# Performance work log

Measured on AMD Instinct MI355X. Metric: run time of the kernel, lower is better.

Reference implementation:

```python
import jax, jax.numpy as jnp
import numpy as np

N_NODES = 8192
N_EDGES = 65536
MUL = 16          # multiplicity of 0e and 1o irreps
NB = 16           # num_radial_basis
HID = 16          # num_radial_dimension
MAX_RADIUS = 5.0
SQRT3 = float(np.sqrt(3.0))


def soft_unit_step(x):
    # e3nn.math.soft_unit_step: exp(-1/x) for x>0 else 0 (grad-safe where)
    safe = jnp.where(x > 0, x, 1.0)
    return jnp.where(x > 0, jnp.exp(-1.0 / safe), 0.0)


def setup_inputs() -> dict:
    key = jax.random.key(0)
    ks = jax.random.split(key, 12)
    f_in = jax.random.normal(ks[0], (N_NODES, 4 * MUL), jnp.float32)
    edge_vec = jax.random.normal(ks[1], (N_EDGES, 3), jnp.float32) * 1.5
    edge_src = jax.random.randint(ks[2], (N_EDGES,), 0, N_NODES)
    edge_dst = jax.random.randint(ks[3], (N_EDGES,), 0, N_NODES)
    Wq0 = jax.random.normal(ks[4], (MUL, MUL), jnp.float32)
    Wq1 = jax.random.normal(ks[5], (MUL, MUL), jnp.float32)
    Wk1 = jax.random.normal(ks[6], (NB, HID), jnp.float32)
    Wk2 = jax.random.normal(ks[7], (HID, 4 * MUL * MUL), jnp.float32)
    Wv1 = jax.random.normal(ks[8], (NB, HID), jnp.float32)
    Wv2 = jax.random.normal(ks[9], (HID, 4 * MUL * MUL), jnp.float32)
    Wd0 = jax.random.normal(ks[10], (MUL, MUL), jnp.float32)
    Wd1 = jax.random.normal(ks[11], (MUL, MUL), jnp.float32)
    return dict(f_in=f_in, edge_vec=edge_vec, edge_src=edge_src, edge_dst=edge_dst,
                Wq0=Wq0, Wq1=Wq1, Wk1=Wk1, Wk2=Wk2, Wv1=Wv1, Wv2=Wv2, Wd0=Wd0, Wd1=Wd1)


def _forward(f_in, edge_vec, edge_src, edge_dst,
             Wq0, Wq1, Wk1, Wk2, Wv1, Wv2, Wd0, Wd1):
    f0 = f_in[:, :MUL]                         # [N, MUL]    0e scalars
    f1 = f_in[:, MUL:].reshape(-1, MUL, 3)     # [N, MUL, 3] 1o vectors

    r = jnp.linalg.norm(edge_vec, axis=1)      # [E]
    u = edge_vec / r[:, None]
    sh1 = SQRT3 * u                            # Y_1, component norm (|Y1|^2 = 3); Y_0 = 1

    # soft_one_hot_linspace, basis='smooth_finite', cutoff=True, * sqrt(NB)
    values = jnp.linspace(0.0, MAX_RADIUS, NB + 2)
    step = values[1] - values[0]
    diff = (r[:, None] - values[1:-1]) / step
    C = 1.14136 * float(np.exp(2.0))
    rb = (C * soft_unit_step(diff + 1.0) * soft_unit_step(1.0 - diff)) * np.sqrt(NB)

    edge_cut = soft_unit_step(10.0 * (1.0 - r / MAX_RADIUS))  # [E]

    def mlp(x, W1, W2):  # e3nn FullyConnectedNet with fan-in normalization
        h = jax.nn.silu(x @ (W1 / np.sqrt(NB)))
        return h @ (W2 / np.sqrt(HID))

    wk = mlp(rb, Wk1, Wk2).reshape(-1, 4, MUL, MUL)  # per-edge TP weights
    wv = mlp(rb, Wv1, Wv2).reshape(-1, 4, MUL, MUL)

    # h_q: per-irrep linear
    q0 = f0 @ Wq0 / np.sqrt(MUL)
    q1 = jnp.einsum('nic,io->noc', f1, Wq1) / np.sqrt(MUL)

    x0 = f0[edge_src]   # [E, MUL]
    x1 = f1[edge_src]   # [E, MUL, 3]

    def fctp(w):
        # FullyConnectedTensorProduct (16x0e+16x1o) x (0e+1o) -> (16x0e+16x1o)
        # 4 paths: 0x0->0, 1x1->0 (dot/sqrt3), 0x1->1, 1x0->1
        a = 1.0 / np.sqrt(2 * MUL)
        o0 = jnp.einsum('eij,ei->ej', w[:, 0], x0) \
           + jnp.einsum('eij,eic,ec->ej', w[:, 1], x1, sh1) / SQRT3
        o1 = jnp.einsum('eij,ei,ec->ejc', w[:, 2], x0, sh1) \
           + jnp.einsum('eij,eic->ejc', w[:, 3], x1)
        return o0 * a, o1 * a

    k0, k1 = fctp(wk)
    v0, v1 = fctp(wv)

    # dot_product: FCTP(query, key) -> 0e
    ad = 1.0 / np.sqrt(2.0 * MUL * MUL)
    dot = ad * (jnp.einsum('ij,ei,ej->e', Wd0, q0[edge_dst], k0)
                + jnp.einsum('ij,eic,ejc->e', Wd1, q1[edge_dst], k1) / SQRT3)

    exp = edge_cut * jnp.exp(dot)                                   # [E]
    z = jax.ops.segment_sum(exp, edge_dst, num_segments=N_NODES)    # [N]
    z = jnp.where(z == 0.0, 1.0, z)
    alpha = exp / z[edge_dst]
    # alpha.relu().sqrt() with grad-safe sqrt at 0
    s = jnp.where(alpha > 0, jnp.sqrt(jnp.where(alpha > 0, alpha, 1.0)), 0.0)

    f_out0 = jax.ops.segment_sum(s[:, None] * v0, edge_dst, num_segments=N_NODES)
    f_out1 = jax.ops.segment_sum(s[:, None, None] * v1, edge_dst, num_segments=N_NODES)
    return jnp.concatenate([f_out0, f_out1.reshape(-1, MUL * 3)], axis=-1)  # [N, 64]


def reference(f_in, edge_vec, edge_src, edge_dst,
              Wq0, Wq1, Wk1, Wk2, Wv1, Wv2, Wd0, Wd1):
    return _forward(f_in, edge_vec, edge_src, edge_dst,
                    Wq0, Wq1, Wk1, Wk2, Wv1, Wv2, Wd0, Wd1)
```

## Files before the change

kernel.cpp:

```cpp
#include <hip/hip_runtime.h>
#include <hip/hip_bf16.h>

#define N_NODES 8192
#define N_EDGES 65536

#define CNT_OFF  0
#define RP_OFF   8192
#define WF_OFF   16640
#define QD0_OFF  33024
#define QD1_OFF  164096
#define EXP_OFF  557312
#define VH_OFF   622848

typedef _Float16 half8 __attribute__((ext_vector_type(8)));
typedef float f32x4 __attribute__((ext_vector_type(4)));

__device__ __forceinline__ float sus_f(float x) { return x > 0.f ? expf(-1.f / x) : 0.f; }
__device__ __forceinline__ float silu_f(float x) { return x / (1.f + expf(-x)); }

__device__ __forceinline__ half8 vmul(half8 v, _Float16 s) {
    half8 r;
#pragma unroll
    for (int d = 0; d < 8; ++d) r[d] = v[d] * s;
    return r;
}

__global__ __launch_bounds__(256) void k_prep(
    const float* __restrict__ f_in,
    const float* __restrict__ Wq0, const float* __restrict__ Wq1,
    const float* __restrict__ Wd0, const float* __restrict__ Wd1,
    const float* __restrict__ Wk2, const float* __restrict__ Wv2,
    const int* __restrict__ edst,
    half8* __restrict__ wfrag, float* __restrict__ qd0, float* __restrict__ qd1,
    int* __restrict__ cnt) {
    __shared__ float f0s[16][16];
    __shared__ float f1s[16][48];
    __shared__ float t0s[16][16];
    __shared__ float t1s[16][48];
    const int blk = blockIdx.x;
    const int tid = threadIdx.x;

    if (blk < 16) {
        int g = blk * 256 + tid;
        int lane = g & 63, t = (g >> 6) & 7, b = (g >> 9) & 3, kv = g >> 11;
        const float* src = kv ? Wv2 : Wk2;
        int n = lane & 15, quad = lane >> 4;
        const float SC = 0.044194173824159216f;
        half8 out;
#pragma unroll
        for (int d = 0; d < 8; ++d) {
            int k = t * 32 + quad * 8 + d;
            int i = k & 15, h = k >> 4;
            out[d] = (_Float16)(src[h * 1024 + b * 256 + i * 16 + n] * SC);
        }
        wfrag[g] = out;
        return;
    }
    if (blk >= 528) {
        int base = (blk - 528) * 256 + tid;
#pragma unroll
        for (int k = 0; k < 4; ++k) atomicAdd(cnt + edst[base + k * 16384], 1);
        return;
    }
    const int j = tid & 15, ln = tid >> 4;
    const int n = (blk - 16) * 16 + ln;
    f0s[ln][j]         = f_in[n * 64 + j];
    f1s[ln][j * 3 + 0] = f_in[n * 64 + 16 + j * 3 + 0];
    f1s[ln][j * 3 + 1] = f_in[n * 64 + 16 + j * 3 + 1];
    f1s[ln][j * 3 + 2] = f_in[n * 64 + 16 + j * 3 + 2];
    __syncthreads();
    float t0 = 0.f, ta = 0.f, tb = 0.f, tc = 0.f;
#pragma unroll
    for (int p = 0; p < 16; ++p) {
        float wq0 = Wq0[p * 16 + j];
        float wq1 = Wq1[p * 16 + j];
        t0 += f0s[ln][p] * wq0;
        ta += f1s[ln][p * 3 + 0] * wq1;
        tb += f1s[ln][p * 3 + 1] * wq1;
        tc += f1s[ln][p * 3 + 2] * wq1;
    }
    t0s[ln][j] = t0;
    t1s[ln][j * 3 + 0] = ta; t1s[ln][j * 3 + 1] = tb; t1s[ln][j * 3 + 2] = tc;
    __syncthreads();
    float q0a = 0.f, qa = 0.f, qb = 0.f, qc = 0.f;
#pragma unroll
    for (int i = 0; i < 16; ++i) {
        float wd0 = Wd0[i * 16 + j];
        float wd1 = Wd1[i * 16 + j];
        q0a += t0s[ln][i] * wd0;
        qa  += t1s[ln][i * 3 + 0] * wd1;
        qb  += t1s[ln][i * 3 + 1] * wd1;
        qc  += t1s[ln][i * 3 + 2] * wd1;
    }
    const float S0 = 0.011048543456f;
    const float S1 = 0.0063788674817f;
    qd0[n * 16 + j] = q0a * S0;
    qd1[0 * 131072 + n * 16 + j] = qa * S1;
    qd1[1 * 131072 + n * 16 + j] = qb * S1;
    qd1[2 * 131072 + n * 16 + j] = qc * S1;
}

__global__ __launch_bounds__(1024) void k_scan(int* __restrict__ cnt, int* __restrict__ rowptr) {
    __shared__ int wsum[16];
    __shared__ int woff[16];
    const int t = threadIdx.x;
    const int lane = t & 63, wv = t >> 6;
    const int base = t * 8;
    int v[8]; int s = 0;
    int4 p0 = ((const int4*)cnt)[t * 2];
    int4 p1 = ((const int4*)cnt)[t * 2 + 1];
    v[0] = p0.x; v[1] = p0.y; v[2] = p0.z; v[3] = p0.w;
    v[4] = p1.x; v[5] = p1.y; v[6] = p1.z; v[7] = p1.w;
#pragma unroll
    for (int i = 0; i < 8; ++i) s += v[i];
    int own = s;
#pragma unroll
    for (int off = 1; off < 64; off <<= 1) {
        int u = __shfl_up(s, off);
        if (lane >= off) s += u;
    }
    if (lane == 63) wsum[wv] = s;
    __syncthreads();
    if (wv == 0 && lane < 16) {
        int u = wsum[lane];
        int sc = u;
#pragma unroll
        for (int off = 1; off < 16; off <<= 1) {
            int x = __shfl_up(sc, off);
            if (lane >= off) sc += x;
        }
        woff[lane] = sc - u;
    }
    __syncthreads();
    int run = woff[wv] + (s - own);
#pragma unroll
    for (int i = 0; i < 8; ++i) { rowptr[base + i] = run; cnt[base + i] = run; run += v[i]; }
    if (t == 1023) rowptr[8192] = run;
}

__global__ __launch_bounds__(256) void k_edge(
    const float* __restrict__ f_in, const float* __restrict__ evec,
    const int* __restrict__ esrc, const int* __restrict__ edst,
    const float* __restrict__ Wk1, const float* __restrict__ Wv1,
    const half8* __restrict__ wfrag,
    const float* __restrict__ qd0, const float* __restrict__ qd1,
    int* __restrict__ cursor, float* __restrict__ expbuf, _Float16* __restrict__ vh) {
    __shared__ __align__(16) char s_arena[19456];
    _Float16 (*s_x0h)[24] = (_Float16(*)[24])(s_arena);
    _Float16 (*s_xsh)[24] = (_Float16(*)[24])(s_arena + 3072);
    _Float16 (*s_x1h0)[24] = (_Float16(*)[24])(s_arena + 6144);
    _Float16 (*s_x1h1)[24] = (_Float16(*)[24])(s_arena + 9216);
    _Float16 (*s_x1h2)[24] = (_Float16(*)[24])(s_arena + 12288);
    _Float16 (*s_hkh)[16] = (_Float16(*)[16])(s_arena + 15360);
    _Float16 (*s_hvh)[16] = (_Float16(*)[16])(s_arena + 17408);
    _Float16 (*s_vt)[72]  = (_Float16(*)[72])(s_arena);
    __shared__ float s_rb[64][16];
    __shared__ float s_sh[64][4];
    __shared__ int   s_slot[64];

    const int tid = threadIdx.x;
    const int e0 = blockIdx.x * 64;

    {
        const int el = tid >> 2, q = tid & 3;
        const int e = e0 + el;
        float v0 = evec[e * 3 + 0];
        float v1 = evec[e * 3 + 1];
        float v2 = evec[e * 3 + 2];
        float r = sqrtf(v0 * v0 + v1 * v1 + v2 * v2);
        float rs = r * 3.4f;
#pragma unroll
        for (int bb = 0; bb < 4; ++bb) {
            int b = q * 4 + bb;
            s_rb[el][b] = 33.734292f * sus_f(rs - (float)b) * sus_f((float)(b + 2) - rs);
        }
        if (q == 0) {
            float inv = r > 0.f ? 1.f / r : 0.f;
            const float SQ3 = 1.7320508075688772f;
            s_sh[el][0] = SQ3 * v0 * inv;
            s_sh[el][1] = SQ3 * v1 * inv;
            s_sh[el][2] = SQ3 * v2 * inv;
            s_sh[el][3] = sus_f(10.f - 2.f * r);
        }
    }
    __syncthreads();

    {
        const int j = tid & 15, slot = tid >> 4;
#pragma unroll
        for (int s = 0; s < 4; ++s) {
            const int el = slot * 4 + s;
            const int e = e0 + el;
            float aK = 0.f, aV = 0.f;
#pragma unroll
            for (int b = 0; b < 16; ++b) {
                float rbv = s_rb[el][b];
                aK += rbv * Wk1[b * 16 + j];
                aV += rbv * Wv1[b * 16 + j];
            }
            s_hkh[el][(j & 1) * 8 + (j >> 1)] = (_Float16)silu_f(aK * 0.25f);
            s_hvh[el][(j & 1) * 8 + (j >> 1)] = (_Float16)silu_f(aV * 0.25f);
            const int src = esrc[e];
            float x0 = f_in[src * 64 + j];
            float xa = f_in[src * 64 + 16 + j * 3 + 0];
            float xb = f_in[src * 64 + 16 + j * 3 + 1];
            float xc = f_in[src * 64 + 16 + j * 3 + 2];
            s_x0h[el][j] = (_Float16)x0;
            s_x1h0[el][j] = (_Float16)xa;
            s_x1h1[el][j] = (_Float16)xb;
            s_x1h2[el][j] = (_Float16)xc;
            s_xsh[el][j] = (_Float16)((xa * s_sh[el][0] + xb * s_sh[el][1] + xc * s_sh[el][2])
                                      * 0.57735026919f);
        }
    }
    __syncthreads();

    const int lane = tid & 63;
    const int wv = tid >> 6;
    const int m = lane & 15, quad = lane >> 4;
    const int eb = wv * 16;
    const int eloc = eb + m;
    const int ihalf = quad >> 1;
    const int hh = (quad & 1) * 8;

    half8 X0 = *(const half8*)&s_x0h[eloc][hh];
    half8 XS = *(const half8*)&s_xsh[eloc][hh];
    half8 Xa = *(const half8*)&s_x1h0[eloc][hh];
    half8 Xb = *(const half8*)&s_x1h1[eloc][hh];
    half8 Xc = *(const half8*)&s_x1h2[eloc][hh];
    half8 HK = *(const half8*)&s_hkh[eloc][ihalf * 8];
    half8 HV = *(const half8*)&s_hvh[eloc][ihalf * 8];
    __syncthreads();

    {
        f32x4 o0 = {0.f, 0.f, 0.f, 0.f}, a1 = o0, ax = o0, ay = o0, az = o0;
#pragma unroll
        for (int t = 0; t < 8; ++t) {
            _Float16 hs = HK[t];
            half8 B0 = wfrag[(0 * 8 + t) * 64 + lane];
            half8 B1 = wfrag[(1 * 8 + t) * 64 + lane];
            half8 B2 = wfrag[(2 * 8 + t) * 64 + lane];
            half8 B3 = wfrag[(3 * 8 + t) * 64 + lane];
            half8 A0 = vmul(X0, hs);
            half8 As = vmul(XS, hs);
            half8 Aa = vmul(Xa, hs);
            half8 Ab = vmul(Xb, hs);
            half8 Ac = vmul(Xc, hs);
            o0 = __builtin_amdgcn_mfma_f32_16x16x32_f16(A0, B0, o0, 0, 0, 0);
            o0 = __builtin_amdgcn_mfma_f32_16x16x32_f16(As, B1, o0, 0, 0, 0);
            a1 = __builtin_amdgcn_mfma_f32_16x16x32_f16(A0, B2, a1, 0, 0, 0);
            ax = __builtin_amdgcn_mfma_f32_16x16x32_f16(Aa, B3, ax, 0, 0, 0);
            ay = __builtin_amdgcn_mfma_f32_16x16x32_f16(Ab, B3, ay, 0, 0, 0);
            az = __builtin_amdgcn_mfma_f32_16x16x32_f16(Ac, B3, az, 0, 0, 0);
        }
        const int j = m;
#pragma unroll
        for (int r = 0; r < 4; ++r) {
            const int el = eb + quad * 4 + r;
            const int e = e0 + el;
            const int dst = edst[e];
            float sh0 = s_sh[el][0], sh1 = s_sh[el][1], sh2 = s_sh[el][2];
            float k1x = a1[r] * sh0 + ax[r];
            float k1y = a1[r] * sh1 + ay[r];
            float k1z = a1[r] * sh2 + az[r];
            float dp = qd0[dst * 16 + j] * o0[r]
                     + qd1[0 * 131072 + dst * 16 + j] * k1x
                     + qd1[1 * 131072 + dst * 16 + j] * k1y
                     + qd1[2 * 131072 + dst * 16 + j] * k1z;
            dp += __shfl_xor(dp, 1);
            dp += __shfl_xor(dp, 2);
            dp += __shfl_xor(dp, 4);
            dp += __shfl_xor(dp, 8);
            if (j == 0) {
                float ev = s_sh[el][3] * expf(dp);
                int slot = atomicAdd(cursor + dst, 1);
                s_slot[el] = slot;
                expbuf[slot] = ev;
            }
        }
    }

    {
        f32x4 o0 = {0.f, 0.f, 0.f, 0.f}, a1 = o0, ax = o0, ay = o0, az = o0;
        const half8* wfv = wfrag + 32 * 64;
#pragma unroll
        for (int t = 0; t < 8; ++t) {
            _Float16 hs = HV[t];
            half8 B0 = wfv[(0 * 8 + t) * 64 + lane];
            half8 B1 = wfv[(1 * 8 + t) * 64 + lane];
            half8 B2 = wfv[(2 * 8 + t) * 64 + lane];
            half8 B3 = wfv[(3 * 8 + t) * 64 + lane];
            half8 A0 = vmul(X0, hs);
            half8 As = vmul(XS, hs);
            half8 Aa = vmul(Xa, hs);
            half8 Ab = vmul(Xb, hs);
            half8 Ac = vmul(Xc, hs);
            o0 = __builtin_amdgcn_mfma_f32_16x16x32_f16(A0, B0, o0, 0, 0, 0);
            o0 = __builtin_amdgcn_mfma_f32_16x16x32_f16(As, B1, o0, 0, 0, 0);
            a1 = __builtin_amdgcn_mfma_f32_16x16x32_f16(A0, B2, a1, 0, 0, 0);
            ax = __builtin_amdgcn_mfma_f32_16x16x32_f16(Aa, B3, ax, 0, 0, 0);
            ay = __builtin_amdgcn_mfma_f32_16x16x32_f16(Ab, B3, ay, 0, 0, 0);
            az = __builtin_amdgcn_mfma_f32_16x16x32_f16(Ac, B3, az, 0, 0, 0);
        }
        const int j = m;
#pragma unroll
        for (int r = 0; r < 4; ++r) {
            const int el = eb + quad * 4 + r;
            float sh0 = s_sh[el][0], sh1 = s_sh[el][1], sh2 = s_sh[el][2];
            s_vt[el][j] = (_Float16)o0[r];
            s_vt[el][16 + j * 3 + 0] = (_Float16)(a1[r] * sh0 + ax[r]);
            s_vt[el][16 + j * 3 + 1] = (_Float16)(a1[r] * sh1 + ay[r]);
            s_vt[el][16 + j * 3 + 2] = (_Float16)(a1[r] * sh2 + az[r]);
        }
    }
    __syncthreads();

#pragma unroll
    for (int pass = 0; pass < 2; ++pass) {
        int row = pass * 32 + (tid >> 3);
        int part = tid & 7;
        half8 val = *(const half8*)&s_vt[row][part * 8];
        int slot = s_slot[row];
        *(half8*)(vh + (size_t)slot * 64 + part * 8) = val;
    }
}

__global__ __launch_bounds__(256) void k_out(
    const int* __restrict__ rowptr,
    const float* __restrict__ expbuf, const _Float16* __restrict__ vh,
    float* __restrict__ fout) {
    const int col = threadIdx.x & 63;
    const int n = blockIdx.x * 4 + (threadIdx.x >> 6);
    const int s0 = rowptr[n], s1 = rowptr[n + 1];
    float zs = 0.f;
    for (int p = s0 + col; p < s1; p += 64) zs += expbuf[p];
#pragma unroll
    for (int off = 32; off > 0; off >>= 1) zs += __shfl_xor(zs, off);
    float zinv = zs > 0.f ? 1.f / zs : 0.f;
    float acc = 0.f;
    for (int p = s0; p < s1; ++p) {
        float ev = expbuf[p];
        float s = ev > 0.f ? sqrtf(ev * zinv) : 0.f;
        acc += s * (float)vh[(size_t)p * 64 + col];
    }
    fout[n * 64 + col] = acc;
}

extern "C" void kernel_launch(void* const* d_in, const int* in_sizes, int n_in,
                              void* d_out, int out_size, void* d_ws, size_t ws_size,
                              hipStream_t stream) {
    const float* f_in = (const float*)d_in[0];
    const float* evec = (const float*)d_in[1];
    const int* esrc = (const int*)d_in[2];
    const int* edst = (const int*)d_in[3];
    const float* Wq0 = (const float*)d_in[4];
    const float* Wq1 = (const float*)d_in[5];
    const float* Wk1 = (const float*)d_in[6];
    const float* Wk2 = (const float*)d_in[7];
    const float* Wv1 = (const float*)d_in[8];
    const float* Wv2 = (const float*)d_in[9];
    const float* Wd0 = (const float*)d_in[10];
    const float* Wd1 = (const float*)d_in[11];

    float* ws     = (float*)d_ws;
    int*   cnt    = (int*)(ws + CNT_OFF);
    int*   rowptr = (int*)(ws + RP_OFF);
    half8* wfrag  = (half8*)(ws + WF_OFF);
    float* qd0    = ws + QD0_OFF;
    float* qd1    = ws + QD1_OFF;
    float* expb   = ws + EXP_OFF;
    _Float16* vh  = (_Float16*)(ws + VH_OFF);
    float* fout   = (float*)d_out;

    hipMemsetAsync(cnt, 0, (size_t)8192 * sizeof(int), stream);

    k_prep<<<592, 256, 0, stream>>>(f_in, Wq0, Wq1, Wd0, Wd1, Wk2, Wv2, edst,
                                    wfrag, qd0, qd1, cnt);
    k_scan<<<1, 1024, 0, stream>>>(cnt, rowptr);
    k_edge<<<N_EDGES / 64, 256, 0, stream>>>(f_in, evec, esrc, edst, Wk1, Wv1,
                                             wfrag, qd0, qd1, cnt, expb, vh);
    k_out<<<N_NODES / 4, 256, 0, stream>>>(rowptr, expb, vh, fout);
}
```

Before: 121.0 us.

## Fuse histogram and scan into prep, interleave query layout, single-pass output

Drops the memset and the separate scan kernel: one block of k_prep builds the destination histogram in shared memory and scans it, while the other blocks compute the query projections. Query coefficients are stored interleaved as float4, so each edge does one vector load instead of four scattered loads. k_out now accumulates the normaliser and the weighted sum in a single pass, using sqrt(ev)*rsqrt(z), and expf calls become the fast __expf. The single histogram block serialises 65536 shared-memory atomics and may end up on the critical path, and the fast exp slightly changes accuracy.

```diff
diff --git a/kernel.cpp b/kernel.cpp
--- a/kernel.cpp
+++ b/kernel.cpp
@@ -7,16 +7,15 @@
 #define CNT_OFF  0
 #define RP_OFF   8192
 #define WF_OFF   16640
-#define QD0_OFF  33024
-#define QD1_OFF  164096
+#define QDI_OFF  33024
 #define EXP_OFF  557312
 #define VH_OFF   622848
 
 typedef _Float16 half8 __attribute__((ext_vector_type(8)));
 typedef float f32x4 __attribute__((ext_vector_type(4)));
 
-__device__ __forceinline__ float sus_f(float x) { return x > 0.f ? expf(-1.f / x) : 0.f; }
-__device__ __forceinline__ float silu_f(float x) { return x / (1.f + expf(-x)); }
+__device__ __forceinline__ float sus_f(float x) { return x > 0.f ? __expf(-1.f / x) : 0.f; }
+__device__ __forceinline__ float silu_f(float x) { return x / (1.f + __expf(-x)); }
 
 __device__ __forceinline__ half8 vmul(half8 v, _Float16 s) {
     half8 r;
@@ -31,12 +30,14 @@
     const float* __restrict__ Wd0, const float* __restrict__ Wd1,
     const float* __restrict__ Wk2, const float* __restrict__ Wv2,
     const int* __restrict__ edst,
-    half8* __restrict__ wfrag, float* __restrict__ qd0, float* __restrict__ qd1,
-    int* __restrict__ cnt) {
+    half8* __restrict__ wfrag, float* __restrict__ qdi,
+    int* __restrict__ cnt, int* __restrict__ rowptr) {
+    __shared__ int hist[8192];
     __shared__ float f0s[16][16];
     __shared__ float f1s[16][48];
     __shared__ float t0s[16][16];
     __shared__ float t1s[16][48];
+    __shared__ int wbase_s[4];
     const int blk = blockIdx.x;
     const int tid = threadIdx.x;
 
@@ -56,10 +57,43 @@
         wfrag[g] = out;
         return;
     }
-    if (blk >= 528) {
-        int base = (blk - 528) * 256 + tid;
-#pragma unroll
-        for (int k = 0; k < 4; ++k) atomicAdd(cnt + edst[base + k * 16384], 1);
+    if (blk == 528) {
+#pragma unroll
+        for (int i = 0; i < 32; ++i) hist[tid * 32 + i] = 0;
+        __syncthreads();
+        const int4* e4 = (const int4*)edst;
+        for (int i = 0; i < 64; ++i) {
+            int4 v = e4[i * 256 + tid];
+            atomicAdd(&hist[v.x], 1);
+            atomicAdd(&hist[v.y], 1);
+            atomicAdd(&hist[v.z], 1);
+            atomicAdd(&hist[v.w], 1);
+        }
+        __syncthreads();
+        int s = 0;
+#pragma unroll
+        for (int i = 0; i < 32; ++i) s += hist[tid * 32 + i];
+        int own = s;
+        const int lane = tid & 63, wv = tid >> 6;
+#pragma unroll
+        for (int off = 1; off < 64; off <<= 1) {
+            int u = __shfl_up(s, off);
+            if (lane >= off) s += u;
+        }
+        if (lane == 63) wbase_s[wv] = s;
+        __syncthreads();
+        int wb = 0;
+#pragma unroll
+        for (int w = 0; w < 4; ++w) if (w < wv) wb += wbase_s[w];
+        int run = wb + (s - own);
+#pragma unroll
+        for (int i = 0; i < 32; ++i) {
+            int idx = tid * 32 + i;
+            rowptr[idx] = run;
+            cnt[idx] = run;
+            run += hist[idx];
+        }
+        if (tid == 255) rowptr[8192] = run;
         return;
     }
     const int j = tid & 15, ln = tid >> 4;
@@ -94,48 +128,8 @@
     }
     const float S0 = 0.011048543456f;
     const float S1 = 0.0063788674817f;
-    qd0[n * 16 + j] = q0a * S0;
-    qd1[0 * 131072 + n * 16 + j] = qa * S1;
-    qd1[1 * 131072 + n * 16 + j] = qb * S1;
-    qd1[2 * 131072 + n * 16 + j] = qc * S1;
-}
-
-__global__ __launch_bounds__(1024) void k_scan(int* __restrict__ cnt, int* __restrict__ rowptr) {
-    __shared__ int wsum[16];
-    __shared__ int woff[16];
-    const int t = threadIdx.x;
-    const int lane = t & 63, wv = t >> 6;
-    const int base = t * 8;
-    int v[8]; int s = 0;
-    int4 p0 = ((const int4*)cnt)[t * 2];
-    int4 p1 = ((const int4*)cnt)[t * 2 + 1];
-    v[0] = p0.x; v[1] = p0.y; v[2] = p0.z; v[3] = p0.w;
-    v[4] = p1.x; v[5] = p1.y; v[6] = p1.z; v[7] = p1.w;
-#pragma unroll
-    for (int i = 0; i < 8; ++i) s += v[i];
-    int own = s;
-#pragma unroll
-    for (int off = 1; off < 64; off <<= 1) {
-        int u = __shfl_up(s, off);
-        if (lane >= off) s += u;
-    }
-    if (lane == 63) wsum[wv] = s;
-    __syncthreads();
-    if (wv == 0 && lane < 16) {
-        int u = wsum[lane];
-        int sc = u;
-#pragma unroll
-        for (int off = 1; off < 16; off <<= 1) {
-            int x = __shfl_up(sc, off);
-            if (lane >= off) sc += x;
-        }
-        woff[lane] = sc - u;
-    }
-    __syncthreads();
-    int run = woff[wv] + (s - own);
-#pragma unroll
-    for (int i = 0; i < 8; ++i) { rowptr[base + i] = run; cnt[base + i] = run; run += v[i]; }
-    if (t == 1023) rowptr[8192] = run;
+    float4 q = {q0a * S0, qa * S1, qb * S1, qc * S1};
+    ((float4*)qdi)[n * 16 + j] = q;
 }
 
 __global__ __launch_bounds__(256) void k_edge(
@@ -143,7 +137,7 @@
     const int* __restrict__ esrc, const int* __restrict__ edst,
     const float* __restrict__ Wk1, const float* __restrict__ Wv1,
     const half8* __restrict__ wfrag,
-    const float* __restrict__ qd0, const float* __restrict__ qd1,
+    const float* __restrict__ qdi,
     int* __restrict__ cursor, float* __restrict__ expbuf, _Float16* __restrict__ vh) {
     __shared__ __align__(16) char s_arena[19456];
     _Float16 (*s_x0h)[24] = (_Float16(*)[24])(s_arena);
@@ -263,16 +257,14 @@
             float k1x = a1[r] * sh0 + ax[r];
             float k1y = a1[r] * sh1 + ay[r];
             float k1z = a1[r] * sh2 + az[r];
-            float dp = qd0[dst * 16 + j] * o0[r]
-                     + qd1[0 * 131072 + dst * 16 + j] * k1x
-                     + qd1[1 * 131072 + dst * 16 + j] * k1y
-                     + qd1[2 * 131072 + dst * 16 + j] * k1z;
+            float4 q = ((const float4*)qdi)[dst * 16 + j];
+            float dp = q.x * o0[r] + q.y * k1x + q.z * k1y + q.w * k1z;
             dp += __shfl_xor(dp, 1);
             dp += __shfl_xor(dp, 2);
             dp += __shfl_xor(dp, 4);
             dp += __shfl_xor(dp, 8);
             if (j == 0) {
-                float ev = s_sh[el][3] * expf(dp);
+                float ev = s_sh[el][3] * __expf(dp);
                 int slot = atomicAdd(cursor + dst, 1);
                 s_slot[el] = slot;
                 expbuf[slot] = ev;
@@ -333,17 +325,14 @@
     const int n = blockIdx.x * 4 + (threadIdx.x >> 6);
     const int s0 = rowptr[n], s1 = rowptr[n + 1];
     float zs = 0.f;
-    for (int p = s0 + col; p < s1; p += 64) zs += expbuf[p];
-#pragma unroll
-    for (int off = 32; off > 0; off >>= 1) zs += __shfl_xor(zs, off);
-    float zinv = zs > 0.f ? 1.f / zs : 0.f;
     float acc = 0.f;
     for (int p = s0; p < s1; ++p) {
         float ev = expbuf[p];
-        float s = ev > 0.f ? sqrtf(ev * zinv) : 0.f;
-        acc += s * (float)vh[(size_t)p * 64 + col];
-    }
-    fout[n * 64 + col] = acc;
+        zs += ev;
+        acc += sqrtf(ev) * (float)vh[(size_t)p * 64 + col];
+    }
+    float scale = zs > 0.f ? rsqrtf(zs) : 0.f;
+    fout[n * 64 + col] = acc * scale;
 }
 
 extern "C" void kernel_launch(void* const* d_in, const int* in_sizes, int n_in,
@@ -366,18 +355,14 @@
     int*   cnt    = (int*)(ws + CNT_OFF);
     int*   rowptr = (int*)(ws + RP_OFF);
     half8* wfrag  = (half8*)(ws + WF_OFF);
-    float* qd0    = ws + QD0_OFF;
-    float* qd1    = ws + QD1_OFF;
+    float* qdi    = ws + QDI_OFF;
     float* expb   = ws + EXP_OFF;
     _Float16* vh  = (_Float16*)(ws + VH_OFF);
     float* fout   = (float*)d_out;
 
-    hipMemsetAsync(cnt, 0, (size_t)8192 * sizeof(int), stream);
-
-    k_prep<<<592, 256, 0, stream>>>(f_in, Wq0, Wq1, Wd0, Wd1, Wk2, Wv2, edst,
-                                    wfrag, qd0, qd1, cnt);
-    k_scan<<<1, 1024, 0, stream>>>(cnt, rowptr);
+    k_prep<<<529, 256, 0, stream>>>(f_in, Wq0, Wq1, Wd0, Wd1, Wk2, Wv2, edst,
+                                    wfrag, qdi, cnt, rowptr);
     k_edge<<<N_EDGES / 64, 256, 0, stream>>>(f_in, evec, esrc, edst, Wk1, Wv1,
-                                             wfrag, qd0, qd1, cnt, expb, vh);
+                                             wfrag, qdi, cnt, expb, vh);
     k_out<<<N_NODES / 4, 256, 0, stream>>>(rowptr, expb, vh, fout);
 }
```

Result: slower. 133.9 us (+10.7%).

## Interleave query tensors, vectorize gathers, use fast exp, single-pass softmax output

Applied to the files above, without the earlier changes.

Stores the four per-node query components interleaved as float4 so each edge does one 16-byte load instead of four scattered loads, and gathers source features as one float4 per lane with a shared-memory transpose followed by an extra barrier. It swaps expf for the __expf intrinsic. It also merges the normalization sum and the weighted accumulation in the output kernel into one pass, scaling by rsqrt(z) at the end. The fast exp lowers accuracy somewhat, and the extra sync adds a little latency in the edge kernel.

```diff
diff --git a/kernel.cpp b/kernel.cpp
--- a/kernel.cpp
+++ b/kernel.cpp
@@ -7,16 +7,15 @@
 #define CNT_OFF  0
 #define RP_OFF   8192
 #define WF_OFF   16640
-#define QD0_OFF  33024
-#define QD1_OFF  164096
+#define QDI_OFF  33024
 #define EXP_OFF  557312
 #define VH_OFF   622848
 
 typedef _Float16 half8 __attribute__((ext_vector_type(8)));
 typedef float f32x4 __attribute__((ext_vector_type(4)));
 
-__device__ __forceinline__ float sus_f(float x) { return x > 0.f ? expf(-1.f / x) : 0.f; }
-__device__ __forceinline__ float silu_f(float x) { return x / (1.f + expf(-x)); }
+__device__ __forceinline__ float sus_f(float x) { return x > 0.f ? __expf(-1.f / x) : 0.f; }
+__device__ __forceinline__ float silu_f(float x) { return x / (1.f + __expf(-x)); }
 
 __device__ __forceinline__ half8 vmul(half8 v, _Float16 s) {
     half8 r;
@@ -31,7 +30,7 @@
     const float* __restrict__ Wd0, const float* __restrict__ Wd1,
     const float* __restrict__ Wk2, const float* __restrict__ Wv2,
     const int* __restrict__ edst,
-    half8* __restrict__ wfrag, float* __restrict__ qd0, float* __restrict__ qd1,
+    half8* __restrict__ wfrag, float* __restrict__ qdi,
     int* __restrict__ cnt) {
     __shared__ float f0s[16][16];
     __shared__ float f1s[16][48];
@@ -94,10 +93,8 @@
     }
     const float S0 = 0.011048543456f;
     const float S1 = 0.0063788674817f;
-    qd0[n * 16 + j] = q0a * S0;
-    qd1[0 * 131072 + n * 16 + j] = qa * S1;
-    qd1[1 * 131072 + n * 16 + j] = qb * S1;
-    qd1[2 * 131072 + n * 16 + j] = qc * S1;
+    float4 q = {q0a * S0, qa * S1, qb * S1, qc * S1};
+    ((float4*)qdi)[n * 16 + j] = q;
 }
 
 __global__ __launch_bounds__(1024) void k_scan(int* __restrict__ cnt, int* __restrict__ rowptr) {
@@ -143,7 +140,7 @@
     const int* __restrict__ esrc, const int* __restrict__ edst,
     const float* __restrict__ Wk1, const float* __restrict__ Wv1,
     const half8* __restrict__ wfrag,
-    const float* __restrict__ qd0, const float* __restrict__ qd1,
+    const float* __restrict__ qdi,
     int* __restrict__ cursor, float* __restrict__ expbuf, _Float16* __restrict__ vh) {
     __shared__ __align__(16) char s_arena[19456];
     _Float16 (*s_x0h)[24] = (_Float16(*)[24])(s_arena);
@@ -187,6 +184,7 @@
 
     {
         const int j = tid & 15, slot = tid >> 4;
+        _Float16* xp = (_Float16*)(s_arena + 6144);
 #pragma unroll
         for (int s = 0; s < 4; ++s) {
             const int el = slot * 4 + s;
@@ -201,14 +199,32 @@
             s_hkh[el][(j & 1) * 8 + (j >> 1)] = (_Float16)silu_f(aK * 0.25f);
             s_hvh[el][(j & 1) * 8 + (j >> 1)] = (_Float16)silu_f(aV * 0.25f);
             const int src = esrc[e];
-            float x0 = f_in[src * 64 + j];
-            float xa = f_in[src * 64 + 16 + j * 3 + 0];
-            float xb = f_in[src * 64 + 16 + j * 3 + 1];
-            float xc = f_in[src * 64 + 16 + j * 3 + 2];
-            s_x0h[el][j] = (_Float16)x0;
-            s_x1h0[el][j] = (_Float16)xa;
-            s_x1h1[el][j] = (_Float16)xb;
-            s_x1h2[el][j] = (_Float16)xc;
+            float4 v4 = ((const float4*)f_in)[src * 16 + j];
+            if (j < 4) {
+#pragma unroll
+                for (int d = 0; d < 4; ++d)
+                    s_x0h[el][j * 4 + d] = (_Float16)((&v4.x)[d]);
+            } else {
+                const int cc = j * 4 - 16;
+#pragma unroll
+                for (int d = 0; d < 4; ++d) {
+                    int c = cc + d;
+                    int i = c / 3, comp = c - 3 * i;
+                    xp[comp * 1536 + el * 24 + i] = (_Float16)((&v4.x)[d]);
+                }
+            }
+        }
+    }
+    __syncthreads();
+
+    {
+        const int j = tid & 15, slot = tid >> 4;
+#pragma unroll
+        for (int s = 0; s < 4; ++s) {
+            const int el = slot * 4 + s;
+            float xa = (float)s_x1h0[el][j];
+            float xb = (float)s_x1h1[el][j];
+            float xc = (float)s_x1h2[el][j];
             s_xsh[el][j] = (_Float16)((xa * s_sh[el][0] + xb * s_sh[el][1] + xc * s_sh[el][2])
                                       * 0.57735026919f);
         }
@@ -263,16 +279,14 @@
             float k1x = a1[r] * sh0 + ax[r];
             float k1y = a1[r] * sh1 + ay[r];
             float k1z = a1[r] * sh2 + az[r];
-            float dp = qd0[dst * 16 + j] * o0[r]
-                     + qd1[0 * 131072 + dst * 16 + j] * k1x
-                     + qd1[1 * 131072 + dst * 16 + j] * k1y
-                     + qd1[2 * 131072 + dst * 16 + j] * k1z;
+            float4 q = ((const float4*)qdi)[dst * 16 + j];
+            float dp = q.x * o0[r] + q.y * k1x + q.z * k1y + q.w * k1z;
             dp += __shfl_xor(dp, 1);
             dp += __shfl_xor(dp, 2);
             dp += __shfl_xor(dp, 4);
             dp += __shfl_xor(dp, 8);
             if (j == 0) {
-                float ev = s_sh[el][3] * expf(dp);
+                float ev = s_sh[el][3] * __expf(dp);
                 int slot = atomicAdd(cursor + dst, 1);
                 s_slot[el] = slot;
                 expbuf[slot] = ev;
@@ -333,17 +347,14 @@
     const int n = blockIdx.x * 4 + (threadIdx.x >> 6);
     const int s0 = rowptr[n], s1 = rowptr[n + 1];
     float zs = 0.f;
-    for (int p = s0 + col; p < s1; p += 64) zs += expbuf[p];
-#pragma unroll
-    for (int off = 32; off > 0; off >>= 1) zs += __shfl_xor(zs, off);
-    float zinv = zs > 0.f ? 1.f / zs : 0.f;
     float acc = 0.f;
     for (int p = s0; p < s1; ++p) {
         float ev = expbuf[p];
-        float s = ev > 0.f ? sqrtf(ev * zinv) : 0.f;
-        acc += s * (float)vh[(size_t)p * 64 + col];
-    }
-    fout[n * 64 + col] = acc;
+        zs += ev;
+        acc += sqrtf(ev) * (float)vh[(size_t)p * 64 + col];
+    }
+    float scale = zs > 0.f ? rsqrtf(zs) : 0.f;
+    fout[n * 64 + col] = acc * scale;
 }
 
 extern "C" void kernel_launch(void* const* d_in, const int* in_sizes, int n_in,
@@ -366,8 +377,7 @@
     int*   cnt    = (int*)(ws + CNT_OFF);
     int*   rowptr = (int*)(ws + RP_OFF);
     half8* wfrag  = (half8*)(ws + WF_OFF);
-    float* qd0    = ws + QD0_OFF;
-    float* qd1    = ws + QD1_OFF;
+    float* qdi    = ws + QDI_OFF;
     float* expb   = ws + EXP_OFF;
     _Float16* vh  = (_Float16*)(ws + VH_OFF);
     float* fout   = (float*)d_out;
@@ -375,9 +385,9 @@
     hipMemsetAsync(cnt, 0, (size_t)8192 * sizeof(int), stream);
 
     k_prep<<<592, 256, 0, stream>>>(f_in, Wq0, Wq1, Wd0, Wd1, Wk2, Wv2, edst,
-                                    wfrag, qd0, qd1, cnt);
+                                    wfrag, qdi, cnt);
     k_scan<<<1, 1024, 0, stream>>>(cnt, rowptr);
     k_edge<<<N_EDGES / 64, 256, 0, stream>>>(f_in, evec, esrc, edst, Wk1, Wv1,
-                                             wfrag, qd0, qd1, cnt, expb, vh);
+                                             wfrag, qdi, cnt, expb, vh);
     k_out<<<N_NODES / 4, 256, 0, stream>>>(rowptr, expb, vh, fout);
 }
```

Measured after the change: 116.6 us. 3.6% less time.
